# Performance work log

Measured on AMD Instinct MI355X. Metric: run time of the kernel, lower is better.

The kernel has to match this reference:

```python
import jax, jax.numpy as jnp
import numpy as np

COORD = 2
C_IN = 64
C_OUT = 4
PROJ_HID = 256
N_LAT = 4096
N_QRY = 16384
B = 4
E0 = 262144
E1 = 524288
KERNEL_DIMS = [2 * COORD, 64, 64, C_IN]  # LinearChannelMLP layers for the GNO kernel


def _init_linear(key, d_in, d_out):
    kw, kb = jax.random.split(key)
    scale = 1.0 / np.sqrt(d_in)
    W = jax.random.uniform(kw, (d_in, d_out), jnp.float32, -scale, scale)
    b = jax.random.uniform(kb, (d_out,), jnp.float32, -scale, scale)
    return W, b


def setup_inputs() -> dict:
    key = jax.random.key(0)
    ks = jax.random.split(key, 16)
    inp = {
        "latent_tokens_coord": jax.random.uniform(ks[0], (N_LAT, COORD), jnp.float32),
        "rndata": jax.random.normal(ks[1], (B, N_LAT, C_IN), jnp.float32),
        "query_coord": jax.random.uniform(ks[2], (N_QRY, COORD), jnp.float32),
        "src0": jax.random.randint(ks[3], (E0,), 0, N_LAT, jnp.int32),
        "qry0": jnp.sort(jax.random.randint(ks[4], (E0,), 0, N_QRY, jnp.int32)),
        "src1": jax.random.randint(ks[5], (E1,), 0, N_LAT, jnp.int32),
        "qry1": jnp.sort(jax.random.randint(ks[6], (E1,), 0, N_QRY, jnp.int32)),
    }
    # GNO kernel MLP (shared across scales): 4 -> 64 -> 64 -> 64, GELU between layers
    for i in range(3):
        W, b = _init_linear(ks[7 + i], KERNEL_DIMS[i], KERNEL_DIMS[i + 1])
        inp[f"Wk{i}"], inp[f"bk{i}"] = W, b
    # scale-weighting MLP: coord_dim -> 16 -> num_scales, softmax over scales
    inp["Wsw0"], inp["bsw0"] = _init_linear(ks[10], COORD, 16)
    inp["Wsw1"], inp["bsw1"] = _init_linear(ks[11], 16, 2)
    # projection ChannelMLP: in_channels -> 256 -> out_channels, GELU between
    inp["Wp0"], inp["bp0"] = _init_linear(ks[12], C_IN, PROJ_HID)
    inp["Wp1"], inp["bp1"] = _init_linear(ks[13], PROJ_HID, C_OUT)
    return inp


def _kernel_mlp(feat, Wk0, bk0, Wk1, bk1, Wk2, bk2):
    h = jax.nn.gelu(feat @ Wk0 + bk0)
    h = jax.nn.gelu(h @ Wk1 + bk1)
    return h @ Wk2 + bk2  # [E, C_IN]


def _gno_scale(latent_coord, query_coord, rndata, src, qry,
               Wk0, bk0, Wk1, bk1, Wk2, bk2):
    # gather per-edge coords: agg = cat(y_j, x_i) -> kernel MLP -> linear transform k * f_y
    feat = jnp.concatenate([latent_coord[src], query_coord[qry]], axis=-1)  # [E, 2*COORD]
    k = _kernel_mlp(feat, Wk0, bk0, Wk1, bk1, Wk2, bk2)                     # [E, C_IN]
    fy = rndata[:, src, :]                                                  # [B, E, C_IN]
    m = (k[None, :, :] * fy).transpose(1, 0, 2)                             # [E, B, C_IN]
    s = jax.ops.segment_sum(m, qry, num_segments=N_QRY)                     # [Q, B, C_IN]
    cnt = jax.ops.segment_sum(jnp.ones_like(qry, dtype=m.dtype), qry, num_segments=N_QRY)
    mean = s / jnp.maximum(cnt, 1.0)[:, None, None]                         # mean reduction
    return mean.transpose(1, 0, 2)                                          # [B, Q, C_IN]


def reference(latent_tokens_coord, rndata, query_coord,
              src0, qry0, src1, qry1,
              Wk0, bk0, Wk1, bk1, Wk2, bk2,
              Wsw0, bsw0, Wsw1, bsw1,
              Wp0, bp0, Wp1, bp1):
    d0 = _gno_scale(latent_tokens_coord, query_coord, rndata, src0, qry0,
                    Wk0, bk0, Wk1, bk1, Wk2, bk2)
    d1 = _gno_scale(latent_tokens_coord, query_coord, rndata, src1, qry1,
                    Wk0, bk0, Wk1, bk1, Wk2, bk2)
    # scale weights from query coords: softmax over scales
    h = jax.nn.relu(query_coord @ Wsw0 + bsw0)
    w = jax.nn.softmax(h @ Wsw1 + bsw1, axis=-1)          # [Q, 2]
    decoded = w[None, :, 0, None] * d0 + w[None, :, 1, None] * d1  # [B, Q, C_IN]
    # projection ChannelMLP (pointwise over nodes)
    out = jax.nn.gelu(decoded @ Wp0 + bp0) @ Wp1 + bp1    # [B, Q, C_OUT]
    return out
```

## Files before the change

kernel.cpp:

```cpp
#include <hip/hip_runtime.h>
#include <hip/hip_bf16.h>
#include <cstdint>

#define NLAT 4096
#define NQRY 16384
#define QPW  2
#define WPB  4
#define HSTR 68

#define WSYNC() asm volatile("s_waitcnt lgkmcnt(0)" ::: "memory")

typedef __attribute__((ext_vector_type(8))) short bh8;
typedef __attribute__((ext_vector_type(4))) float f32x4;

union FI { int i[4]; int4 q; bh8 v; };


__device__ __forceinline__ float gelu_fast(float x) {
    float x3 = __fmul_rn(__fmul_rn(x, x), x);
    float s  = __fadd_rn(x, __fmul_rn(0.044715f, x3));
    float u2 = __fmul_rn(1.5957691216057308f, s);
    float e  = __expf(u2);
    float r  = __builtin_amdgcn_rcpf(__fadd_rn(e, 1.0f));
    return __fmul_rn(x, __fsub_rn(1.0f, r));
}
__device__ __forceinline__ float gelu_prec(float x) {
    float x3 = __fmul_rn(__fmul_rn(x, x), x);
    float s  = __fadd_rn(x, __fmul_rn(0.044715f, x3));
    float u2 = __fmul_rn(1.5957691216057308f, s);
    float e  = expf(u2);
    return __fmul_rn(x, __fdiv_rn(e, __fadd_rn(e, 1.0f)));
}

__device__ __forceinline__ int lower_bound(const int* __restrict__ a, int n, int v) {
    int lo = 0, hi = n;
    while (lo < hi) { int m = (lo + hi) >> 1; if (a[m] < v) lo = m + 1; else hi = m; }
    return lo;
}

__device__ __forceinline__ int pk(float a, float b) {
    return (int)__builtin_amdgcn_perm(__float_as_uint(b), __float_as_uint(a), 0x07060302u);
}
__device__ __forceinline__ float mask16(float x) {
    return __uint_as_float(__float_as_uint(x) & 0xFFFF0000u);
}

__device__ __forceinline__ void make_afrags(const float* sh, int lane, FI ah[2], FI al[2]) {
    const int m = lane & 15, quad = lane >> 4;
#pragma unroll
    for (int ks = 0; ks < 2; ks++) {
        const float* p = sh + m * HSTR + ks * 32 + quad * 8;
        float4 v0 = *(const float4*)p;
        float4 v1 = *(const float4*)(p + 4);
        float x[8] = {v0.x, v0.y, v0.z, v0.w, v1.x, v1.y, v1.z, v1.w};
#pragma unroll
        for (int jj = 0; jj < 4; jj++) {
            float a = x[2 * jj], b = x[2 * jj + 1];
            ah[ks].i[jj] = pk(a, b);
            float la = __fsub_rn(a, mask16(a));
            float lb = __fsub_rn(b, mask16(b));
            al[ks].i[jj] = pk(la, lb);
        }
    }
}

__global__ __launch_bounds__(WPB * 64, 3) void fused_kernel(
    const float* __restrict__ lat,  const float* __restrict__ rnd,
    const float* __restrict__ qc,
    const int* __restrict__ src0, const int* __restrict__ qry0, int E0,
    const int* __restrict__ src1, const int* __restrict__ qry1, int E1,
    const float* __restrict__ Wk0, const float* __restrict__ bk0,
    const float* __restrict__ Wk1, const float* __restrict__ bk1,
    const float* __restrict__ Wk2, const float* __restrict__ bk2,
    const float* __restrict__ Wsw0, const float* __restrict__ bsw0,
    const float* __restrict__ Wsw1, const float* __restrict__ bsw1,
    const float* __restrict__ Wp0, const float* __restrict__ bp0,
    const float* __restrict__ Wp1, const float* __restrict__ bp1,
    float* __restrict__ out)
{
    const int lane = threadIdx.x & 63;
    const int wid  = threadIdx.x >> 6;
    const int m16  = lane & 15;
    const int quad = lane >> 4;

    __shared__ __align__(16) float sh_all[WPB][16 * HSTR];
    __shared__ __align__(16) float decs_all[WPB][4][64];
    __shared__ __align__(16) int4  wlds[2][2][4][2][64];
    float* __restrict__ sh = sh_all[wid];
    float (* __restrict__ decs)[64] = decs_all[wid];

    if (wid == 0) {
        const float* Wmat[2] = {Wk1, Wk2};
#pragma unroll
        for (int L = 0; L < 2; L++)
#pragma unroll
            for (int ks = 0; ks < 2; ks++)
#pragma unroll
                for (int nt = 0; nt < 4; nt++) {
                    FI fh, fl;
#pragma unroll
                    for (int jj = 0; jj < 4; jj++) {
                        int k0 = ks * 32 + quad * 8 + 2 * jj;
                        float a = Wmat[L][(size_t)k0 * 64 + nt * 16 + m16];
                        float b = Wmat[L][(size_t)(k0 + 1) * 64 + nt * 16 + m16];
                        fh.i[jj] = pk(a, b);
                        float la = __fsub_rn(a, mask16(a));
                        float lb = __fsub_rn(b, mask16(b));
                        fl.i[jj] = pk(la, lb);
                    }
                    wlds[L][ks][nt][0][lane] = fh.q;
                    wlds[L][ks][nt][1][lane] = fl.q;
                }
    }

    const float w00 = Wk0[0 * 64 + lane];
    const float w01 = Wk0[1 * 64 + lane];
    const float w02 = Wk0[2 * 64 + lane];
    const float w03 = Wk0[3 * 64 + lane];
    const float b0  = bk0[lane];
    float b1v[4], b2v[4];
#pragma unroll
    for (int nt = 0; nt < 4; nt++) {
        b1v[nt] = bk1[16 * nt + m16];
        b2v[nt] = bk2[16 * nt + m16];
    }

    __syncthreads();

    const int qbase = (blockIdx.x * WPB + wid) * QPW;
    int bs = 0;
    {
        const bool in0 = lane < 3;
        const bool act = lane < 6;
        const int* arr = in0 ? qry0 : qry1;
        const int  n   = in0 ? E0 : E1;
        const int  v   = qbase + (in0 ? lane : lane - 3);
        if (act) bs = lower_bound(arr, n, v);
    }

    for (int qi = 0; qi < QPW; qi++) {
        const int q = qbase + qi;
        const float qc0 = qc[2 * q];
        const float qc1 = qc[2 * q + 1];

        const int lo0 = __shfl(bs, qi, 64),     hi0 = __shfl(bs, qi + 1, 64);
        const int lo1 = __shfl(bs, 3 + qi, 64), hi1 = __shfl(bs, 4 + qi, 64);

        int pS[2] = {0, 0}; float pl0[2] = {0.f, 0.f}, pl1[2] = {0.f, 0.f};
#pragma unroll
        for (int s = 0; s < 2; s++) {
            const int lo = s ? lo1 : lo0, hi = s ? hi1 : hi0;
            const int* sp = s ? src1 : src0;
            if (lo < hi) {
                int idx = lo + m16; if (idx >= hi) idx = hi - 1;
                pS[s]  = sp[idx];
                pl0[s] = lat[2 * pS[s]];
                pl1[s] = lat[2 * pS[s] + 1];
            }
        }

        float msum[2][4];

#pragma unroll
        for (int set = 0; set < 2; set++) {
            const int* __restrict__ srcp = set ? src1 : src0;
            const int lo = set ? lo1 : lo0;
            const int hi = set ? hi1 : hi0;
            float a0 = 0.f, a1 = 0.f, a2 = 0.f, a3 = 0.f;

            int curS = pS[set]; float curl0 = pl0[set], curl1 = pl1[set];

            for (int e0 = lo; e0 < hi; e0 += 16) {
                const int rem = min(16, hi - e0);

                int nS = 0; float nl0 = 0.f, nl1 = 0.f;
                if (e0 + 16 < hi) {
                    int idx = e0 + 16 + m16; if (idx >= hi) idx = hi - 1;
                    nS  = srcp[idx];
                    nl0 = lat[2 * nS];
                    nl1 = lat[2 * nS + 1];
                }

#pragma unroll
                for (int e = 0; e < 16; e++) {
                    float l0 = __shfl(curl0, e, 64);
                    float l1 = __shfl(curl1, e, 64);
                    float t  = __fmul_rn(l0, w00);
                    t = __fmaf_rn(l1,  w01, t);
                    t = __fmaf_rn(qc0, w02, t);
                    t = __fmaf_rn(qc1, w03, t);
                    t = __fadd_rn(t, b0);
                    sh[e * HSTR + lane] = gelu_fast(t);
                }
                WSYNC();

                FI ah[2], al[2];
                make_afrags(sh, lane, ah, al);
                WSYNC();

#pragma unroll
                for (int nt = 0; nt < 4; nt++) {
                    f32x4 C = {0.f, 0.f, 0.f, 0.f};
#pragma unroll
                    for (int ks = 0; ks < 2; ks++) {
                        FI fh, fl;
                        fh.q = wlds[0][ks][nt][0][lane];
                        fl.q = wlds[0][ks][nt][1][lane];
                        C = __builtin_amdgcn_mfma_f32_16x16x32_bf16(ah[ks].v, fh.v, C, 0, 0, 0);
                        C = __builtin_amdgcn_mfma_f32_16x16x32_bf16(al[ks].v, fh.v, C, 0, 0, 0);
                        C = __builtin_amdgcn_mfma_f32_16x16x32_bf16(ah[ks].v, fl.v, C, 0, 0, 0);
                        C = __builtin_amdgcn_mfma_f32_16x16x32_bf16(al[ks].v, fl.v, C, 0, 0, 0);
                    }
#pragma unroll
                    for (int r = 0; r < 4; r++)
                        sh[(quad * 4 + r) * HSTR + 16 * nt + m16] =
                            gelu_fast(__fadd_rn(C[r], b1v[nt]));
                }
                WSYNC();

                float rA[8][4];
#pragma unroll
                for (int e = 0; e < 8; e++) {
                    const int s = __shfl(curS, e, 64);
                    const float* rp = rnd + (size_t)s * 64 + lane;
                    rA[e][0] = rp[0];
                    rA[e][1] = rp[(size_t)1 * NLAT * 64];
                    rA[e][2] = rp[(size_t)2 * NLAT * 64];
                    rA[e][3] = rp[(size_t)3 * NLAT * 64];
                }

                make_afrags(sh, lane, ah, al);
                WSYNC();

#pragma unroll
                for (int nt = 0; nt < 4; nt++) {
                    f32x4 C = {0.f, 0.f, 0.f, 0.f};
#pragma unroll
                    for (int ks = 0; ks < 2; ks++) {
                        FI fh, fl;
                        fh.q = wlds[1][ks][nt][0][lane];
                        fl.q = wlds[1][ks][nt][1][lane];
                        C = __builtin_amdgcn_mfma_f32_16x16x32_bf16(ah[ks].v, fh.v, C, 0, 0, 0);
                        C = __builtin_amdgcn_mfma_f32_16x16x32_bf16(al[ks].v, fh.v, C, 0, 0, 0);
                        C = __builtin_amdgcn_mfma_f32_16x16x32_bf16(ah[ks].v, fl.v, C, 0, 0, 0);
                        C = __builtin_amdgcn_mfma_f32_16x16x32_bf16(al[ks].v, fl.v, C, 0, 0, 0);
                    }
#pragma unroll
                    for (int r = 0; r < 4; r++)
                        sh[(quad * 4 + r) * HSTR + 16 * nt + m16] = __fadd_rn(C[r], b2v[nt]);
                }

                float rB[8][4];
#pragma unroll
                for (int e = 0; e < 8; e++) {
                    const int s = __shfl(curS, 8 + e, 64);
                    const float* rp = rnd + (size_t)s * 64 + lane;
                    rB[e][0] = rp[0];
                    rB[e][1] = rp[(size_t)1 * NLAT * 64];
                    rB[e][2] = rp[(size_t)2 * NLAT * 64];
                    rB[e][3] = rp[(size_t)3 * NLAT * 64];
                }
                WSYNC();

                float kvv[16];
#pragma unroll
                for (int e = 0; e < 16; e++) {
                    const float v = sh[e * HSTR + lane];
                    kvv[e] = (e < rem) ? v : 0.f;
                }

#pragma unroll
                for (int e = 0; e < 8; e++) {
                    a0 = __fadd_rn(a0, __fmul_rn(kvv[e], rA[e][0]));
                    a1 = __fadd_rn(a1, __fmul_rn(kvv[e], rA[e][1]));
                    a2 = __fadd_rn(a2, __fmul_rn(kvv[e], rA[e][2]));
                    a3 = __fadd_rn(a3, __fmul_rn(kvv[e], rA[e][3]));
                }
#pragma unroll
                for (int e = 0; e < 8; e++) {
                    a0 = __fadd_rn(a0, __fmul_rn(kvv[8 + e], rB[e][0]));
                    a1 = __fadd_rn(a1, __fmul_rn(kvv[8 + e], rB[e][1]));
                    a2 = __fadd_rn(a2, __fmul_rn(kvv[8 + e], rB[e][2]));
                    a3 = __fadd_rn(a3, __fmul_rn(kvv[8 + e], rB[e][3]));
                }
                WSYNC();

                curS = nS; curl0 = nl0; curl1 = nl1;
            }

            const float cntf = fmaxf((float)(hi - lo), 1.0f);
            msum[set][0] = __fdiv_rn(a0, cntf);
            msum[set][1] = __fdiv_rn(a1, cntf);
            msum[set][2] = __fdiv_rn(a2, cntf);
            msum[set][3] = __fdiv_rn(a3, cntf);
        }

        float z0a = 0.f, z1a = 0.f;
#pragma unroll
        for (int i = 0; i < 16; i++) {
            float t = __fmul_rn(qc0, Wsw0[i]);
            t = __fmaf_rn(qc1, Wsw0[16 + i], t);
            t = __fadd_rn(t, bsw0[i]);
            const float h = fmaxf(0.f, t);
            z0a = __fmaf_rn(h, Wsw1[i * 2 + 0], z0a);
            z1a = __fmaf_rn(h, Wsw1[i * 2 + 1], z1a);
        }
        const float z0 = __fadd_rn(z0a, bsw1[0]);
        const float z1 = __fadd_rn(z1a, bsw1[1]);
        const float zm = fmaxf(z0, z1);
        const float e0s = expf(__fsub_rn(z0, zm)), e1s = expf(__fsub_rn(z1, zm));
        const float s01 = __fadd_rn(e0s, e1s);
        const float g0 = __fdiv_rn(e0s, s01), g1 = __fdiv_rn(e1s, s01);

        WSYNC();
#pragma unroll
        for (int b = 0; b < 4; b++)
            decs[b][lane] = __fadd_rn(__fmul_rn(g0, msum[0][b]),
                                      __fmul_rn(g1, msum[1][b]));
        WSYNC();

        float hacc[4][4];
#pragma unroll
        for (int t = 0; t < 4; t++)
#pragma unroll
            for (int b = 0; b < 4; b++) hacc[t][b] = 0.f;
#pragma unroll 8
        for (int c = 0; c < 64; c++) {
            const float4 w = ((const float4*)Wp0)[c * 64 + lane];
            const float wf[4] = { w.x, w.y, w.z, w.w };
            const float d0 = decs[0][c], d1 = decs[1][c], d2 = decs[2][c], d3 = decs[3][c];
#pragma unroll
            for (int t = 0; t < 4; t++) {
                hacc[t][0] = __fmaf_rn(wf[t], d0, hacc[t][0]);
                hacc[t][1] = __fmaf_rn(wf[t], d1, hacc[t][1]);
                hacc[t][2] = __fmaf_rn(wf[t], d2, hacc[t][2]);
                hacc[t][3] = __fmaf_rn(wf[t], d3, hacc[t][3]);
            }
        }
        {
            const float4 bv = ((const float4*)bp0)[lane];
            const float bt[4] = { bv.x, bv.y, bv.z, bv.w };
#pragma unroll
            for (int t = 0; t < 4; t++)
#pragma unroll
                for (int b = 0; b < 4; b++)
                    hacc[t][b] = gelu_prec(__fadd_rn(hacc[t][b], bt[t]));
        }

        float po[4][4];
#pragma unroll
        for (int b = 0; b < 4; b++)
#pragma unroll
            for (int k = 0; k < 4; k++) po[b][k] = 0.f;
#pragma unroll
        for (int t = 0; t < 4; t++) {
            const float4 w = ((const float4*)Wp1)[4 * lane + t];
            const float wf[4] = { w.x, w.y, w.z, w.w };
#pragma unroll
            for (int k = 0; k < 4; k++)
#pragma unroll
                for (int b = 0; b < 4; b++)
                    po[b][k] = __fmaf_rn(hacc[t][b], wf[k], po[b][k]);
        }
#pragma unroll
        for (int b = 0; b < 4; b++)
#pragma unroll
            for (int k = 0; k < 4; k++) {
                float v = po[b][k];
#pragma unroll
                for (int off = 32; off >= 1; off >>= 1)
                    v = __fadd_rn(v, __shfl_xor(v, off, 64));
                po[b][k] = v;
            }

        if (lane == 0) {
#pragma unroll
            for (int b = 0; b < 4; b++)
#pragma unroll
                for (int k = 0; k < 4; k++)
                    out[((size_t)b * NQRY + q) * 4 + k] = __fadd_rn(po[b][k], bp1[k]);
        }
        WSYNC();
    }
}

extern "C" void kernel_launch(void* const* d_in, const int* in_sizes, int n_in,
                              void* d_out, int out_size, void* d_ws, size_t ws_size,
                              hipStream_t stream) {
    const float* lat  = (const float*)d_in[0];
    const float* rnd  = (const float*)d_in[1];
    const float* qc   = (const float*)d_in[2];
    const int*   src0 = (const int*)d_in[3];
    const int*   qry0 = (const int*)d_in[4];
    const int*   src1 = (const int*)d_in[5];
    const int*   qry1 = (const int*)d_in[6];
    const float* Wk0 = (const float*)d_in[7],  *bk0 = (const float*)d_in[8];
    const float* Wk1 = (const float*)d_in[9],  *bk1 = (const float*)d_in[10];
    const float* Wk2 = (const float*)d_in[11], *bk2 = (const float*)d_in[12];
    const float* Wsw0 = (const float*)d_in[13], *bsw0 = (const float*)d_in[14];
    const float* Wsw1 = (const float*)d_in[15], *bsw1 = (const float*)d_in[16];
    const float* Wp0 = (const float*)d_in[17], *bp0 = (const float*)d_in[18];
    const float* Wp1 = (const float*)d_in[19], *bp1 = (const float*)d_in[20];

    const int E0 = in_sizes[3];
    const int E1 = in_sizes[5];

    fused_kernel<<<NQRY / (QPW * WPB), WPB * 64, 0, stream>>>(
        lat, rnd, qc, src0, qry0, E0, src1, qry1, E1,
        Wk0, bk0, Wk1, bk1, Wk2, bk2,
        Wsw0, bsw0, Wsw1, bsw1, Wp0, bp0, Wp1, bp1,
        (float*)d_out);
}
```

Before: 345.6 us.

## Precompute CSR bounds, double waves per block, hoist gathers, add MFMA priority

Two small kernels now build per-query segment offsets for both edge lists, replacing the per-wave binary searches over the sorted query arrays. Blocks grow from 4 to 8 waves with a launch bound of 4, and the second batch of rndata gathers is issued before the second MFMA layer instead of after it. The MFMA sections are also bracketed with s_setprio so other waves' loads can issue in the meantime. In exchange the change adds two extra launches and workspace traffic, more LDS per block, and more register pressure from holding both gather buffers at once.

```diff
diff --git a/kernel.cpp b/kernel.cpp
--- a/kernel.cpp
+++ b/kernel.cpp
@@ -5,7 +5,7 @@
 #define NLAT 4096
 #define NQRY 16384
 #define QPW  2
-#define WPB  4
+#define WPB  8
 #define HSTR 68
 
 #define WSYNC() asm volatile("s_waitcnt lgkmcnt(0)" ::: "memory")
@@ -32,12 +32,6 @@
     return __fmul_rn(x, __fdiv_rn(e, __fadd_rn(e, 1.0f)));
 }
 
-__device__ __forceinline__ int lower_bound(const int* __restrict__ a, int n, int v) {
-    int lo = 0, hi = n;
-    while (lo < hi) { int m = (lo + hi) >> 1; if (a[m] < v) lo = m + 1; else hi = m; }
-    return lo;
-}
-
 __device__ __forceinline__ int pk(float a, float b) {
     return (int)__builtin_amdgcn_perm(__float_as_uint(b), __float_as_uint(a), 0x07060302u);
 }
@@ -64,11 +58,23 @@
     }
 }
 
-__global__ __launch_bounds__(WPB * 64, 3) void fused_kernel(
+__global__ __launch_bounds__(256) void build_bounds(
+    const int* __restrict__ qry, int E, int* __restrict__ lb)
+{
+    int i = blockIdx.x * blockDim.x + threadIdx.x;
+    if (i >= E) return;
+    const int c = qry[i];
+    const int p = (i == 0) ? -1 : qry[i - 1];
+    for (int v = p + 1; v <= c; ++v) lb[v] = i;
+    if (i == E - 1)
+        for (int v = c + 1; v <= NQRY; ++v) lb[v] = E;
+}
+
+__global__ __launch_bounds__(WPB * 64, 4) void fused_kernel(
     const float* __restrict__ lat,  const float* __restrict__ rnd,
     const float* __restrict__ qc,
-    const int* __restrict__ src0, const int* __restrict__ qry0, int E0,
-    const int* __restrict__ src1, const int* __restrict__ qry1, int E1,
+    const int* __restrict__ src0, const int* __restrict__ cnt0,
+    const int* __restrict__ src1, const int* __restrict__ cnt1,
     const float* __restrict__ Wk0, const float* __restrict__ bk0,
     const float* __restrict__ Wk1, const float* __restrict__ bk1,
     const float* __restrict__ Wk2, const float* __restrict__ bk2,
@@ -129,14 +135,8 @@
 
     const int qbase = (blockIdx.x * WPB + wid) * QPW;
     int bs = 0;
-    {
-        const bool in0 = lane < 3;
-        const bool act = lane < 6;
-        const int* arr = in0 ? qry0 : qry1;
-        const int  n   = in0 ? E0 : E1;
-        const int  v   = qbase + (in0 ? lane : lane - 3);
-        if (act) bs = lower_bound(arr, n, v);
-    }
+    if (lane < 3)      bs = cnt0[qbase + lane];
+    else if (lane < 6) bs = cnt1[qbase + lane - 3];
 
     for (int qi = 0; qi < QPW; qi++) {
         const int q = qbase + qi;
@@ -198,6 +198,7 @@
                 make_afrags(sh, lane, ah, al);
                 WSYNC();
 
+                __builtin_amdgcn_s_setprio(1);
 #pragma unroll
                 for (int nt = 0; nt < 4; nt++) {
                     f32x4 C = {0.f, 0.f, 0.f, 0.f};
@@ -216,9 +217,10 @@
                         sh[(quad * 4 + r) * HSTR + 16 * nt + m16] =
                             gelu_fast(__fadd_rn(C[r], b1v[nt]));
                 }
-                WSYNC();
-
-                float rA[8][4];
+                __builtin_amdgcn_s_setprio(0);
+                WSYNC();
+
+                float rA[8][4], rB[8][4];
 #pragma unroll
                 for (int e = 0; e < 8; e++) {
                     const int s = __shfl(curS, e, 64);
@@ -228,10 +230,20 @@
                     rA[e][2] = rp[(size_t)2 * NLAT * 64];
                     rA[e][3] = rp[(size_t)3 * NLAT * 64];
                 }
+#pragma unroll
+                for (int e = 0; e < 8; e++) {
+                    const int s = __shfl(curS, 8 + e, 64);
+                    const float* rp = rnd + (size_t)s * 64 + lane;
+                    rB[e][0] = rp[0];
+                    rB[e][1] = rp[(size_t)1 * NLAT * 64];
+                    rB[e][2] = rp[(size_t)2 * NLAT * 64];
+                    rB[e][3] = rp[(size_t)3 * NLAT * 64];
+                }
 
                 make_afrags(sh, lane, ah, al);
                 WSYNC();
 
+                __builtin_amdgcn_s_setprio(1);
 #pragma unroll
                 for (int nt = 0; nt < 4; nt++) {
                     f32x4 C = {0.f, 0.f, 0.f, 0.f};
@@ -249,17 +261,7 @@
                     for (int r = 0; r < 4; r++)
                         sh[(quad * 4 + r) * HSTR + 16 * nt + m16] = __fadd_rn(C[r], b2v[nt]);
                 }
-
-                float rB[8][4];
-#pragma unroll
-                for (int e = 0; e < 8; e++) {
-                    const int s = __shfl(curS, 8 + e, 64);
-                    const float* rp = rnd + (size_t)s * 64 + lane;
-                    rB[e][0] = rp[0];
-                    rB[e][1] = rp[(size_t)1 * NLAT * 64];
-                    rB[e][2] = rp[(size_t)2 * NLAT * 64];
-                    rB[e][3] = rp[(size_t)3 * NLAT * 64];
-                }
+                __builtin_amdgcn_s_setprio(0);
                 WSYNC();
 
                 float kvv[16];
@@ -405,8 +407,14 @@
     const int E0 = in_sizes[3];
     const int E1 = in_sizes[5];
 
+    int* cnt0 = (int*)d_ws;
+    int* cnt1 = cnt0 + (NQRY + 1);
+
+    build_bounds<<<(E0 + 255) / 256, 256, 0, stream>>>(qry0, E0, cnt0);
+    build_bounds<<<(E1 + 255) / 256, 256, 0, stream>>>(qry1, E1, cnt1);
+
     fused_kernel<<<NQRY / (QPW * WPB), WPB * 64, 0, stream>>>(
-        lat, rnd, qc, src0, qry0, E0, src1, qry1, E1,
+        lat, rnd, qc, src0, cnt0, src1, cnt1,
         Wk0, bk0, Wk1, bk1, Wk2, bk2,
         Wsw0, bsw0, Wsw1, bsw1, Wp0, bp0, Wp1, bp1,
         (float*)d_out);
```

Measured after the change: 363.4 us. 5.1% more time.
